# Optimization experiments

Hardware: AMD Instinct MI355X
Metric: run time of the kernel (lower is better)

The kernel has to match this reference:

```python
import jax, jax.numpy as jnp
import numpy as np

N_VERT = 163842  # icosphere level-7 vertex count
IN_FEATS = 64
OUT_FEATS = 64
BATCH = 2
K = 7  # center vertex + 6 one-ring neighbors


def setup_inputs() -> dict:
    key = jax.random.key(0)
    k1, k2, k3, k4 = jax.random.split(key, 4)
    x = jax.random.normal(k1, (N_VERT, IN_FEATS, BATCH), dtype=jnp.float32)
    neigh_orders = jax.random.randint(k2, (K * N_VERT,), 0, N_VERT, dtype=jnp.int64)
    W = jax.random.normal(k3, (OUT_FEATS, K * IN_FEATS), dtype=jnp.float32) * 0.05
    b = jax.random.normal(k4, (OUT_FEATS,), dtype=jnp.float32) * 0.05
    return {"x": x, "neigh_orders": neigh_orders, "W": W, "b": b}


def reference(x, neigh_orders, W, b):
    # x: [N, C, B]; neigh_orders: [7N] flat indices, grouped per-vertex (n*7 + k)
    N = x.shape[0]
    C = x.shape[1]
    idx = neigh_orders.reshape(N, K)            # [N, 7]
    gathered = x[idx]                           # [N, 7, C, B] irregular gather
    Wr = W.reshape(W.shape[0], K, C)            # [O, 7, C] matches flatten order (k*C + c)
    # out[n, o, b] = sum_{k,c} gathered[n,k,c,b] * W[o, k*C + c] + b[o]
    out = jnp.einsum("nkcb,okc->nob", gathered, Wr) + b[None, :, None]
    return out  # [N, O, B]
```

## Files before the change

### kernel.cpp

```cpp
#include <hip/hip_runtime.h>

#define NV      163842
#define CIN     64
#define KN      7
#define NKMAX   (NV * KN)
#define KDIM    448
#define KSTEPS  14
#define VPC     16
#define ROWS    32
#define NSEG    224
#define ABUFS   (NSEG * 64)
#define ASTRIDE 456

typedef short  short8 __attribute__((ext_vector_type(8)));
typedef float  f32x4  __attribute__((ext_vector_type(4)));

static __device__ __forceinline__ unsigned int pack_bf16(float a, float b) {
#if __has_builtin(__builtin_amdgcn_cvt_pk_bf16_f32)
    typedef __bf16 bf16x2 __attribute__((ext_vector_type(2)));
    union { bf16x2 v; unsigned int u; } cv;
    cv.v = __builtin_amdgcn_cvt_pk_bf16_f32(a, b);
    return cv.u;
#else
    unsigned int ua = __float_as_uint(a);
    unsigned int ub = __float_as_uint(b);
    ua = (ua + 0x7FFFu + ((ua >> 16) & 1u)) >> 16;
    ub = (ub + 0x7FFFu + ((ub >> 16) & 1u)) & 0xFFFF0000u;
    return ua | ub;
#endif
}

static __device__ __forceinline__ void bar_lgkm() {
    asm volatile("s_waitcnt lgkmcnt(0)\n\ts_barrier" ::: "memory");
}

#define WAITVM(N) asm volatile("s_waitcnt vmcnt(" #N ")" ::: "memory")

static __device__ __forceinline__ void dma16(const unsigned short* g, unsigned short* l) {
    __builtin_amdgcn_global_load_lds(
        (const __attribute__((address_space(1))) unsigned int*)g,
        (__attribute__((address_space(3))) unsigned int*)l, 16, 0, 0);
}

__global__ __launch_bounds__(256)
void xcast(const float* __restrict__ x, unsigned int* __restrict__ xt, int nf4)
{
    const int f = blockIdx.x * 256 + threadIdx.x;
    if (f >= nf4) return;
    const f32x4 g = __builtin_nontemporal_load(&((const f32x4*)x)[f]);
    const int v = f >> 5;
    const int r = f & 31;
    xt[v * 64 + r]      = pack_bf16(g[0], g[2]);
    xt[v * 64 + 32 + r] = pack_bf16(g[1], g[3]);
}

__global__ __launch_bounds__(256, 2)
void onering_mfma_bf16_v5(const unsigned short* __restrict__ xt,
                          const int* __restrict__ neigh,
                          const float* __restrict__ W,
                          const float* __restrict__ bias,
                          float* __restrict__ out,
                          int nchunks)
{
    __shared__ __align__(16) unsigned short A_lds[2 * ABUFS];
    __shared__ __align__(16) float          C_lds[VPC * 128];

    const int tid  = threadIdx.x;
    const int lane = tid & 63;
    const int w    = tid >> 6;
    const int ncol = lane & 15;
    const int kgrp = lane >> 4;
    const int G    = gridDim.x;

    short8 bfrag[KSTEPS];
    {
        const int o = w * 16 + ncol;
#pragma unroll
        for (int s = 0; s < KSTEPS; ++s) {
            const int kb = s * 32 + kgrp * 8;
            const float4* wp = (const float4*)(W + o * KDIM + kb);
            float4 w0 = wp[0];
            float4 w1 = wp[1];
            union { short8 v; unsigned int u[4]; } pk;
            pk.u[0] = pack_bf16(w0.x, w0.y);
            pk.u[1] = pack_bf16(w0.z, w0.w);
            pk.u[2] = pack_bf16(w1.x, w1.y);
            pk.u[3] = pack_bf16(w1.z, w1.w);
            bfrag[s] = pk.v;
        }
    }
    const float biasv = bias[w * 16 + ncol];

    const int l8 = tid & 7;
    int nidx[7];
    int ldst[7];
    int gso[7];
#pragma unroll
    for (int i = 0; i < 7; ++i) {
        const int seg = (tid >> 3) + 32 * i;
        const int lv  = seg / 14;
        const int rem = seg - lv * 14;
        const int k   = rem >> 1;
        const int bb  = rem & 1;
        nidx[i] = lv * KN + k;
        ldst[i] = seg * 64 + l8 * 8;
        gso[i]  = bb * 64 + ((l8 ^ (seg & 7)) << 3);
    }

    const int ch0 = blockIdx.x;
    int I[7];
    int I2[7];

#pragma unroll
    for (int i = 0; i < 7; ++i) {
        int gi = ch0 * (VPC * KN) + nidx[i];
        I[i] = __builtin_nontemporal_load(&neigh[gi < NKMAX ? gi : 0]);
    }
    WAITVM(0);
#pragma unroll
    for (int i = 0; i < 7; ++i)
        dma16(xt + (size_t)I[i] * 128 + gso[i], A_lds + ldst[i]);
#pragma unroll
    for (int i = 0; i < 7; ++i) {
        int gi = (ch0 + G) * (VPC * KN) + nidx[i];
        I2[i] = __builtin_nontemporal_load(&neigh[gi < NKMAX ? gi : 0]);
    }
    WAITVM(0);
#pragma unroll
    for (int i = 0; i < 7; ++i) I[i] = I2[i];
#pragma unroll
    for (int i = 0; i < 7; ++i) {
        int gi = (ch0 + 2 * G) * (VPC * KN) + nidx[i];
        I2[i] = __builtin_nontemporal_load(&neigh[gi < NKMAX ? gi : 0]);
    }

    int cur = 0;
    for (int ch = ch0; ch < nchunks; ch += G) {
        const int vb = ch * VPC;

        unsigned short* Aw = A_lds + (cur ^ 1) * ABUFS;
#pragma unroll
        for (int i = 0; i < 7; ++i)
            dma16(xt + (size_t)I[i] * 128 + gso[i], Aw + ldst[i]);

        WAITVM(14);
        __builtin_amdgcn_s_barrier();

        WAITVM(7);
#pragma unroll
        for (int i = 0; i < 7; ++i) I[i] = I2[i];
#pragma unroll
        for (int i = 0; i < 7; ++i) {
            int gi = (ch + 3 * G) * (VPC * KN) + nidx[i];
            I2[i] = __builtin_nontemporal_load(&neigh[gi < NKMAX ? gi : 0]);
        }

        const unsigned short* Ab = A_lds + cur * ABUFS;
        const int rb0 = (ncol >> 1) * 14 + (ncol & 1);
        f32x4 acc0 = {0.f, 0.f, 0.f, 0.f};
        f32x4 acc1 = {0.f, 0.f, 0.f, 0.f};
#pragma unroll
        for (int s = 0; s < KSTEPS; ++s) {
            const int p0   = (s & 1) * 4 + kgrp;
            const int seg0 = rb0 + (s >> 1) * 2;
            const int slot = (p0 ^ (seg0 & 7)) << 3;
            const short8 a0 = *(const short8*)&Ab[seg0 * 64 + slot];
            const short8 a1 = *(const short8*)&Ab[(seg0 + 112) * 64 + slot];
            acc0 = __builtin_amdgcn_mfma_f32_16x16x32_bf16(a0, bfrag[s], acc0, 0, 0, 0);
            acc1 = __builtin_amdgcn_mfma_f32_16x16x32_bf16(a1, bfrag[s], acc1, 0, 0, 0);
        }

        const int o2 = (w * 16 + ncol) * 2;
#pragma unroll
        for (int j = 0; j < 4; ++j) {
            const int r  = kgrp * 4 + j;
            C_lds[(r >> 1) * 128 + o2 + (r & 1)] = acc0[j] + biasv;
            const int r2 = 16 + r;
            C_lds[(r2 >> 1) * 128 + o2 + (r2 & 1)] = acc1[j] + biasv;
        }
        bar_lgkm();
        f32x4* dst = (f32x4*)(out + vb * 128);
#pragma unroll
        for (int it = 0; it < 2; ++it) {
            const int fidx = tid + 256 * it;
            if (vb + (fidx >> 5) < NV)
                __builtin_nontemporal_store(((const f32x4*)C_lds)[fidx], &dst[fidx]);
        }

        cur ^= 1;
    }
}

__global__ __launch_bounds__(256, 4)
void onering_mfma_f32(const float* __restrict__ x,
                      const int* __restrict__ neigh,
                      const float* __restrict__ W,
                      const float* __restrict__ bias,
                      float* __restrict__ out,
                      int nchunks)
{
    __shared__ unsigned short A_lds[ROWS * ASTRIDE];
    const int tid  = threadIdx.x;
    const int lane = tid & 63;
    const int w    = tid >> 6;
    const int ncol = lane & 15;
    const int kgrp = lane >> 4;

    short8 bfrag[KSTEPS];
    {
        const int o = w * 16 + ncol;
#pragma unroll
        for (int s = 0; s < KSTEPS; ++s) {
            const int kb = s * 32 + kgrp * 8;
            const float4* wp = (const float4*)(W + o * KDIM + kb);
            float4 w0 = wp[0];
            float4 w1 = wp[1];
            union { short8 v; unsigned int u[4]; } pk;
            pk.u[0] = pack_bf16(w0.x, w0.y);
            pk.u[1] = pack_bf16(w0.z, w0.w);
            pk.u[2] = pack_bf16(w1.x, w1.y);
            pk.u[3] = pack_bf16(w1.z, w1.w);
            bfrag[s] = pk.v;
        }
    }
    const float biasv = bias[w * 16 + ncol];
    const int off4  = tid & 31;
    const int sbase = tid >> 5;

    for (int ch = blockIdx.x; ch < nchunks; ch += gridDim.x) {
        const int vb = ch * VPC;
        __syncthreads();
#pragma unroll
        for (int i = 0; i < 14; ++i) {
            const int s  = sbase + 8 * i;
            const int lv = s / 7;
            const int k  = s - lv * 7;
            const int n  = vb + lv;
            int vi = 0;
            if (n < NV) vi = neigh[n * KN + k];
            const float4 g = ((const float4*)x)[vi * 32 + off4];
            const int base = k * 64 + 2 * off4;
            ((unsigned int*)A_lds)[((lv * 2)     * ASTRIDE + base) >> 1] = pack_bf16(g.x, g.z);
            ((unsigned int*)A_lds)[((lv * 2 + 1) * ASTRIDE + base) >> 1] = pack_bf16(g.y, g.w);
        }
        __syncthreads();
        f32x4 acc0 = {0.f, 0.f, 0.f, 0.f};
        f32x4 acc1 = {0.f, 0.f, 0.f, 0.f};
#pragma unroll
        for (int s = 0; s < KSTEPS; ++s) {
            const int kb = s * 32 + kgrp * 8;
            const short8 a0 = *(const short8*)&A_lds[ncol * ASTRIDE + kb];
            const short8 a1 = *(const short8*)&A_lds[(16 + ncol) * ASTRIDE + kb];
            acc0 = __builtin_amdgcn_mfma_f32_16x16x32_bf16(a0, bfrag[s], acc0, 0, 0, 0);
            acc1 = __builtin_amdgcn_mfma_f32_16x16x32_bf16(a1, bfrag[s], acc1, 0, 0, 0);
        }
        const int o = w * 16 + ncol;
#pragma unroll
        for (int j = 0; j < 4; ++j) {
            const int r = kgrp * 4 + j;
            {
                const int lv = r >> 1, bb = r & 1, n = vb + lv;
                if (n < NV) out[n * 128 + o * 2 + bb] = acc0[j] + biasv;
            }
            {
                const int m = 16 + r;
                const int lv = m >> 1, bb = m & 1, n = vb + lv;
                if (n < NV) out[n * 128 + o * 2 + bb] = acc1[j] + biasv;
            }
        }
    }
}

extern "C" void kernel_launch(void* const* d_in, const int* in_sizes, int n_in,
                              void* d_out, int out_size, void* d_ws, size_t ws_size,
                              hipStream_t stream) {
    const float* x     = (const float*)d_in[0];
    const int*   neigh = (const int*)d_in[1];
    const float* W     = (const float*)d_in[2];
    const float* bias  = (const float*)d_in[3];
    float*       out   = (float*)d_out;

    const int nchunks = (NV + VPC - 1) / VPC;
    const size_t need = (size_t)NV * 128 * sizeof(unsigned short);

    if (ws_size >= need) {
        unsigned short* xt = (unsigned short*)d_ws;
        const int nf4 = NV * 32;
        xcast<<<dim3((nf4 + 255) / 256), dim3(256), 0, stream>>>(x, (unsigned int*)xt, nf4);
        onering_mfma_bf16_v5<<<dim3(512), dim3(256), 0, stream>>>(xt, neigh, W, bias, out, nchunks);
    } else {
        onering_mfma_f32<<<dim3(2560), dim3(256), 0, stream>>>(x, neigh, W, bias, out, nchunks);
    }
}
```

Before: 204.2 us.

## Switch to 32x32x16 MFMA with split-K across waves and shorter index prefetch

The gather-GEMM kernel now uses 32x32x16 bf16 MFMA. Each wave covers 32 output columns over half of the K dimension, and the two K halves are reduced through a new LDS partial buffer with an extra barrier. The neighbor-index prefetch is cut from three chunks ahead to two, which drops the I2 register copy. The aim is fewer LDS A-fragment reads per MFMA and fewer MFMA instructions, at the cost of an added LDS reduction and synchronization step.

```diff
diff --git a/kernel.cpp b/kernel.cpp
--- a/kernel.cpp
+++ b/kernel.cpp
@@ -5,15 +5,16 @@
 #define KN      7
 #define NKMAX   (NV * KN)
 #define KDIM    448
-#define KSTEPS  14
 #define VPC     16
 #define ROWS    32
 #define NSEG    224
 #define ABUFS   (NSEG * 64)
+#define KSTEPS  14
 #define ASTRIDE 456
 
 typedef short  short8 __attribute__((ext_vector_type(8)));
 typedef float  f32x4  __attribute__((ext_vector_type(4)));
+typedef float  f32x16 __attribute__((ext_vector_type(16)));
 
 static __device__ __forceinline__ unsigned int pack_bf16(float a, float b) {
 #if __has_builtin(__builtin_amdgcn_cvt_pk_bf16_f32)
@@ -55,7 +56,7 @@
 }
 
 __global__ __launch_bounds__(256, 2)
-void onering_mfma_bf16_v5(const unsigned short* __restrict__ xt,
+void onering_mfma_bf16_v6(const unsigned short* __restrict__ xt,
                           const int* __restrict__ neigh,
                           const float* __restrict__ W,
                           const float* __restrict__ bias,
@@ -63,22 +64,25 @@
                           int nchunks)
 {
     __shared__ __align__(16) unsigned short A_lds[2 * ABUFS];
+    __shared__ __align__(16) float          P_lds[2 * 1024];
     __shared__ __align__(16) float          C_lds[VPC * 128];
 
     const int tid  = threadIdx.x;
     const int lane = tid & 63;
     const int w    = tid >> 6;
-    const int ncol = lane & 15;
-    const int kgrp = lane >> 4;
+    const int wc   = w & 1;
+    const int kh   = w >> 1;
+    const int col  = lane & 31;
+    const int hi   = lane >> 5;
     const int G    = gridDim.x;
 
     short8 bfrag[KSTEPS];
     {
-        const int o = w * 16 + ncol;
+        const int o   = wc * 32 + col;
+        const int kb0 = kh * 224 + hi * 8;
 #pragma unroll
         for (int s = 0; s < KSTEPS; ++s) {
-            const int kb = s * 32 + kgrp * 8;
-            const float4* wp = (const float4*)(W + o * KDIM + kb);
+            const float4* wp = (const float4*)(W + o * KDIM + kb0 + s * 16);
             float4 w0 = wp[0];
             float4 w1 = wp[1];
             union { short8 v; unsigned int u[4]; } pk;
@@ -89,7 +93,10 @@
             bfrag[s] = pk.v;
         }
     }
-    const float biasv = bias[w * 16 + ncol];
+    const float biasv = bias[wc * 32 + col];
+
+    const int rb  = (col >> 1) * 14 + (col & 1);
+    const int khb = kh * 224 + hi * 8;
 
     const int l8 = tid & 7;
     int nidx[7];
@@ -109,7 +116,6 @@
 
     const int ch0 = blockIdx.x;
     int I[7];
-    int I2[7];
 
 #pragma unroll
     for (int i = 0; i < 7; ++i) {
@@ -123,62 +129,60 @@
 #pragma unroll
     for (int i = 0; i < 7; ++i) {
         int gi = (ch0 + G) * (VPC * KN) + nidx[i];
-        I2[i] = __builtin_nontemporal_load(&neigh[gi < NKMAX ? gi : 0]);
+        I[i] = __builtin_nontemporal_load(&neigh[gi < NKMAX ? gi : 0]);
     }
     WAITVM(0);
-#pragma unroll
-    for (int i = 0; i < 7; ++i) I[i] = I2[i];
-#pragma unroll
-    for (int i = 0; i < 7; ++i) {
-        int gi = (ch0 + 2 * G) * (VPC * KN) + nidx[i];
-        I2[i] = __builtin_nontemporal_load(&neigh[gi < NKMAX ? gi : 0]);
-    }
 
     int cur = 0;
     for (int ch = ch0; ch < nchunks; ch += G) {
         const int vb = ch * VPC;
 
+        WAITVM(2);
+
         unsigned short* Aw = A_lds + (cur ^ 1) * ABUFS;
 #pragma unroll
         for (int i = 0; i < 7; ++i)
             dma16(xt + (size_t)I[i] * 128 + gso[i], Aw + ldst[i]);
 
-        WAITVM(14);
         __builtin_amdgcn_s_barrier();
 
-        WAITVM(7);
-#pragma unroll
-        for (int i = 0; i < 7; ++i) I[i] = I2[i];
 #pragma unroll
         for (int i = 0; i < 7; ++i) {
-            int gi = (ch + 3 * G) * (VPC * KN) + nidx[i];
-            I2[i] = __builtin_nontemporal_load(&neigh[gi < NKMAX ? gi : 0]);
+            int gi = (ch + 2 * G) * (VPC * KN) + nidx[i];
+            I[i] = __builtin_nontemporal_load(&neigh[gi < NKMAX ? gi : 0]);
         }
 
         const unsigned short* Ab = A_lds + cur * ABUFS;
-        const int rb0 = (ncol >> 1) * 14 + (ncol & 1);
-        f32x4 acc0 = {0.f, 0.f, 0.f, 0.f};
-        f32x4 acc1 = {0.f, 0.f, 0.f, 0.f};
+        f32x16 acc = {0.f};
 #pragma unroll
         for (int s = 0; s < KSTEPS; ++s) {
-            const int p0   = (s & 1) * 4 + kgrp;
-            const int seg0 = rb0 + (s >> 1) * 2;
-            const int slot = (p0 ^ (seg0 & 7)) << 3;
-            const short8 a0 = *(const short8*)&Ab[seg0 * 64 + slot];
-            const short8 a1 = *(const short8*)&Ab[(seg0 + 112) * 64 + slot];
-            acc0 = __builtin_amdgcn_mfma_f32_16x16x32_bf16(a0, bfrag[s], acc0, 0, 0, 0);
-            acc1 = __builtin_amdgcn_mfma_f32_16x16x32_bf16(a1, bfrag[s], acc1, 0, 0, 0);
-        }
-
-        const int o2 = (w * 16 + ncol) * 2;
-#pragma unroll
-        for (int j = 0; j < 4; ++j) {
-            const int r  = kgrp * 4 + j;
-            C_lds[(r >> 1) * 128 + o2 + (r & 1)] = acc0[j] + biasv;
-            const int r2 = 16 + r;
-            C_lds[(r2 >> 1) * 128 + o2 + (r2 & 1)] = acc1[j] + biasv;
+            const int kk0  = khb + s * 16;
+            const int k    = kk0 >> 6;
+            const int p    = (kk0 >> 3) & 7;
+            const int seg  = rb + 2 * k;
+            const int slot = (p ^ (seg & 7)) << 3;
+            const short8 a = *(const short8*)&Ab[seg * 64 + slot];
+            acc = __builtin_amdgcn_mfma_f32_32x32x16_bf16(a, bfrag[s], acc, 0, 0, 0);
+        }
+
+        if (kh) {
+#pragma unroll
+            for (int g = 0; g < 16; ++g) {
+                const int row = (g & 3) + 8 * (g >> 2) + 4 * hi;
+                P_lds[wc * 1024 + row * 32 + col] = acc[g];
+            }
         }
         bar_lgkm();
+        if (!kh) {
+#pragma unroll
+            for (int g = 0; g < 16; ++g) {
+                const int row = (g & 3) + 8 * (g >> 2) + 4 * hi;
+                const float v = acc[g] + P_lds[wc * 1024 + row * 32 + col] + biasv;
+                C_lds[(row >> 1) * 128 + (wc * 32 + col) * 2 + (row & 1)] = v;
+            }
+        }
+        bar_lgkm();
+
         f32x4* dst = (f32x4*)(out + vb * 128);
 #pragma unroll
         for (int it = 0; it < 2; ++it) {
@@ -199,6 +203,7 @@
                       float* __restrict__ out,
                       int nchunks)
 {
+    typedef float f32x4l __attribute__((ext_vector_type(4)));
     __shared__ unsigned short A_lds[ROWS * ASTRIDE];
     const int tid  = threadIdx.x;
     const int lane = tid & 63;
@@ -206,11 +211,11 @@
     const int ncol = lane & 15;
     const int kgrp = lane >> 4;
 
-    short8 bfrag[KSTEPS];
+    short8 bfrag[14];
     {
         const int o = w * 16 + ncol;
 #pragma unroll
-        for (int s = 0; s < KSTEPS; ++s) {
+        for (int s = 0; s < 14; ++s) {
             const int kb = s * 32 + kgrp * 8;
             const float4* wp = (const float4*)(W + o * KDIM + kb);
             float4 w0 = wp[0];
@@ -244,10 +249,10 @@
             ((unsigned int*)A_lds)[((lv * 2 + 1) * ASTRIDE + base) >> 1] = pack_bf16(g.y, g.w);
         }
         __syncthreads();
-        f32x4 acc0 = {0.f, 0.f, 0.f, 0.f};
-        f32x4 acc1 = {0.f, 0.f, 0.f, 0.f};
-#pragma unroll
-        for (int s = 0; s < KSTEPS; ++s) {
+        f32x4l acc0 = {0.f, 0.f, 0.f, 0.f};
+        f32x4l acc1 = {0.f, 0.f, 0.f, 0.f};
+#pragma unroll
+        for (int s = 0; s < 14; ++s) {
             const int kb = s * 32 + kgrp * 8;
             const short8 a0 = *(const short8*)&A_lds[ncol * ASTRIDE + kb];
             const short8 a1 = *(const short8*)&A_lds[(16 + ncol) * ASTRIDE + kb];
@@ -287,7 +292,7 @@
         unsigned short* xt = (unsigned short*)d_ws;
         const int nf4 = NV * 32;
         xcast<<<dim3((nf4 + 255) / 256), dim3(256), 0, stream>>>(x, (unsigned int*)xt, nf4);
-        onering_mfma_bf16_v5<<<dim3(512), dim3(256), 0, stream>>>(xt, neigh, W, bias, out, nchunks);
+        onering_mfma_bf16_v6<<<dim3(512), dim3(256), 0, stream>>>(xt, neigh, W, bias, out, nchunks);
     } else {
         onering_mfma_f32<<<dim3(2560), dim3(256), 0, stream>>>(x, neigh, W, bias, out, nchunks);
     }
```

Measured after the change: 202.9 us. No clear change (-0.6%).
